# Kernel tuning notes

Measured on AMD Instinct MI355X. Metric: run time of the kernel, lower is better.

The kernel has to match this reference:

```python
import jax, jax.numpy as jnp
import numpy as np
from jax import lax

NUM_CHANNELS = 64
DILATION_DEPTH = 9
NUM_REPEAT = 2
KERNEL_SIZE = 3
DILATIONS = [2 ** d for d in range(DILATION_DEPTH)] * NUM_REPEAT  # 18 layers
B, T = 4, 32768


def causal_conv1d(x, w, b, dilation):
    # x: [B, Cin, T], w: [Cout, Cin, K], b: [Cout]
    # left-pad by (K-1)*dilation -> causal, output length T
    pad = (w.shape[-1] - 1) * dilation
    out = lax.conv_general_dilated(
        x, w, window_strides=(1,), padding=[(pad, 0)],
        rhs_dilation=(dilation,), dimension_numbers=("NCH", "OIH", "NCH"))
    return out + b[None, :, None]


def setup_inputs() -> dict:
    key = jax.random.key(0)
    ks = jax.random.split(key, 9)
    L, C = len(DILATIONS), NUM_CHANNELS
    s = 0.05
    return {
        "x": jax.random.normal(ks[0], (B, 1, T), dtype=jnp.float32),
        "in_w": jax.random.normal(ks[1], (C, 1, 1), dtype=jnp.float32) * s,
        "in_b": jax.random.normal(ks[2], (C,), dtype=jnp.float32) * s,
        "hid_w": jax.random.normal(ks[3], (L, 2 * C, C, KERNEL_SIZE), dtype=jnp.float32) * s,
        "hid_b": jax.random.normal(ks[4], (L, 2 * C), dtype=jnp.float32) * s,
        "res_w": jax.random.normal(ks[5], (L, C, C, 1), dtype=jnp.float32) * s,
        "res_b": jax.random.normal(ks[6], (L, C), dtype=jnp.float32) * s,
        "mix_w": jax.random.normal(ks[7], (1, L * C, 1), dtype=jnp.float32) * s,
        "mix_b": jax.random.normal(ks[8], (1,), dtype=jnp.float32) * s,
    }


def reference(x, in_w, in_b, hid_w, hid_b, res_w, res_b, mix_w, mix_b):
    C = NUM_CHANNELS
    out = causal_conv1d(x, in_w, in_b, 1)  # [B, C, T]
    skips = []
    for i, d in enumerate(DILATIONS):
        inp = out
        h = causal_conv1d(inp, hid_w[i], hid_b[i], d)  # [B, 2C, T]
        gated = jnp.tanh(h[:, :C]) * jax.nn.sigmoid(h[:, C:])  # [B, C, T]
        skips.append(gated)
        out = causal_conv1d(gated, res_w[i], res_b[i], 1) + inp
    skip_cat = jnp.concatenate(skips, axis=1)  # [B, L*C, T]
    return causal_conv1d(skip_cat, mix_w, mix_b, 1)  # [B, 1, T]
```

## Files before the change

kernel.cpp:

```cpp
#include <hip/hip_runtime.h>
#include <math.h>

#define T_LEN 32768
#define NB 4
#define NC 64
#define NL 18

typedef __attribute__((ext_vector_type(8))) short s16x8;
typedef __attribute__((ext_vector_type(4))) float f32x4;
#define MFMA_F16 __builtin_amdgcn_mfma_f32_16x16x32_f16

#define BAR_LGKM()                                                   \
    do {                                                             \
        asm volatile("s_waitcnt lgkmcnt(0)" ::: "memory");           \
        __builtin_amdgcn_s_barrier();                                \
        __builtin_amdgcn_sched_barrier(0);                           \
    } while (0)
#define BAR_VM(N)                                                    \
    do {                                                             \
        asm volatile("s_waitcnt vmcnt(%0) lgkmcnt(0)" ::             \
                         "i"(N) : "memory");                         \
        __builtin_amdgcn_s_barrier();                                \
        __builtin_amdgcn_sched_barrier(0);                           \
    } while (0)

__device__ inline unsigned short f2h(float f) {
    _Float16 h = (_Float16)f;
    return __builtin_bit_cast(unsigned short, h);
}
__device__ inline unsigned pack_h2(float a, float b) {
    return (unsigned)f2h(a) | ((unsigned)f2h(b) << 16);
}
__device__ inline float h2f(unsigned short u) {
    return (float)__builtin_bit_cast(_Float16, u);
}
__device__ inline float fast_sigmoid(float x) {
    return __builtin_amdgcn_rcpf(1.f + __expf(-x));
}
__device__ inline float fast_tanh(float x) {
    return 1.f - 2.f * __builtin_amdgcn_rcpf(1.f + __expf(2.f * x));
}

__global__ void prep_kernel(const float* __restrict__ hid_w,
                            const float* __restrict__ res_w,
                            const float* __restrict__ mix_b,
                            unsigned short* __restrict__ Wh,
                            unsigned short* __restrict__ Wr,
                            float* __restrict__ out,
                            float* __restrict__ zerobuf) {
    const int nW1 = NL * 128 * 192;
    const int nW2 = NL * 64 * 64;
    const int nOut = NB * T_LEN;
    const int total = nW1 + nW2 + nOut + 48;
    for (int gid = blockIdx.x * blockDim.x + threadIdx.x; gid < total;
         gid += gridDim.x * blockDim.x) {
        if (gid < nW1) {
            int K = gid % 192;
            int co = (gid / 192) & 127;
            int i = gid / (192 * 128);
            int kt = K >> 6, ci = K & 63;
            Wh[gid] = f2h(hid_w[((i * 128 + co) * 64 + ci) * 3 + kt]);
        } else if (gid < nW1 + nW2) {
            int q = gid - nW1;
            int c = q & 63, co = (q >> 6) & 63, i = q >> 12;
            Wr[q] = f2h(res_w[(i * 64 + co) * 64 + c]);
        } else if (gid < nW1 + nW2 + nOut) {
            out[gid - (nW1 + nW2)] = mix_b[0];
        } else {
            zerobuf[gid - (nW1 + nW2 + nOut)] = 0.f;
        }
    }
}

template <int DIL, bool FIRST, bool LAST>
__launch_bounds__(256, 4)
__global__ void layer_kernel(const unsigned short* __restrict__ actH,
                             unsigned short* __restrict__ outH,
                             const unsigned short* __restrict__ Wh,
                             const float* __restrict__ hb,
                             const unsigned short* __restrict__ Wr,
                             const float* __restrict__ rb,
                             const float* __restrict__ mw,
                             float* __restrict__ skip,
                             const float* __restrict__ zerobuf,
                             const float* __restrict__ x,
                             const float* __restrict__ in_w,
                             const float* __restrict__ in_b) {
    constexpr bool UNI = (DIL < 64);
    constexpr int R = UNI ? (64 + 2 * DIL) : 192;
    constexpr int SLOTS = R * 8;
    constexpr int JMAX = (SLOTS + 255) / 256;
    constexpr int GS_BASE = (UNI ? 128 : 0) * 128;
    constexpr int OUT_BASE = (UNI ? 0 : 64) * 128;
    constexpr int REG = 24576;

    __shared__ uint4 Xs[2 * 1536];
    __shared__ float Sk[256];
    char* lds = (char*)Xs;

    const int tid = threadIdx.x;
    const int w = tid >> 6;
    const int l = tid & 63;
    const int lo = l & 15;
    const int hi = l >> 4;
    const int blk = blockIdx.x;
    const int tile = (blk & 7) * 64 + (blk >> 3);
    const int t0 = tile * 64;
    const int m0 = 16 * w;
    const int c0 = m0 + 4 * hi;

    const float* xB0 = x;

    s16x8 AH[2][6];
    s16x8 AR[2];
#pragma unroll
    for (int mt = 0; mt < 2; mt++) {
        const unsigned short* wp = Wh + (size_t)(m0 + 64 * mt + lo) * 192;
#pragma unroll
        for (int s = 0; s < 6; s++)
            AH[mt][s] = *(const s16x8*)(wp + 32 * s + 8 * hi);
    }
    if (!LAST) {
#pragma unroll
        for (int s = 0; s < 2; s++)
            AR[s] = *(const s16x8*)(Wr + (size_t)(m0 + lo) * 64 + 32 * s + 8 * hi);
    }
    float bA[4], bB[4], rbv[4];
#pragma unroll
    for (int r = 0; r < 4; r++) {
        bA[r] = hb[c0 + r];
        bB[r] = hb[64 + c0 + r];
        rbv[r] = LAST ? 0.f : rb[c0 + r];
    }
    const float4 mw4 = *(const float4*)(mw + c0);

    auto stage_async = [&](int bb, char* X) {
        const unsigned short* aB = actH + (size_t)bb * T_LEN * NC;
#pragma unroll
        for (int jj = 0; jj < JMAX; jj++) {
            int s = (w * JMAX + jj) * 64 + l;
            const void* src;
            if (s >= SLOTS) {
                src = (const void*)(zerobuf + (s & 7) * 4);
            } else {
                int row = s >> 3, ch = s & 7;
                int chunk = ch ^ (row & 7);
                int tg = t0 + (UNI ? (row - 2 * DIL)
                                   : (((row >> 6) - 2) * DIL + (row & 63)));
                src = (tg >= 0)
                          ? (const void*)(aB + (size_t)tg * 64 + chunk * 8)
                          : (const void*)(zerobuf + chunk * 4);
            }
            __builtin_amdgcn_global_load_lds(
                (const __attribute__((address_space(1))) unsigned int*)src,
                (__attribute__((address_space(3))) unsigned int*)(X +
                                                        (w * JMAX + jj) * 1024),
                16, 0, 0);
        }
    };
    auto stage_first = [&](int bb, char* X) {
        const float* xB = xB0 + (size_t)bb * T_LEN;
#pragma unroll
        for (int jj = 0; jj < JMAX; jj++) {
            int p = jj * 256 + tid;
            if (p < SLOTS) {
                int row = p >> 3, ch = p & 7;
                int tg = t0 + row - 2 * DIL;
                unsigned uu[4] = {0u, 0u, 0u, 0u};
                if (tg >= 0) {
                    float a = xB[tg];
#pragma unroll
                    for (int e = 0; e < 4; e++) {
                        float v0 = a * in_w[ch * 8 + 2 * e] + in_b[ch * 8 + 2 * e];
                        float v1 = a * in_w[ch * 8 + 2 * e + 1] + in_b[ch * 8 + 2 * e + 1];
                        uu[e] = pack_h2(v0, v1);
                    }
                }
                int byte = (row * 128 + ch * 16) ^ ((row & 7) << 4);
                *(uint4*)(X + byte) = make_uint4(uu[0], uu[1], uu[2], uu[3]);
            }
        }
    };

    if (FIRST) stage_first(0, lds);
    else       stage_async(0, lds);

#pragma unroll
    for (int j = 0; j < NB; j++) {
        char* X = lds + (j & 1) * REG;
        const int b = j;

        if (j + 1 < NB) {
            if (FIRST) stage_first(j + 1, lds + ((j + 1) & 1) * REG);
            else       stage_async(j + 1, lds + ((j + 1) & 1) * REG);
        }

        if (FIRST)           { BAR_LGKM(); }
        else if (j + 1 < NB) { BAR_VM(JMAX); }
        else                 { BAR_VM(0); }

        f32x4 acc[2][4];
#pragma unroll
        for (int mt = 0; mt < 2; mt++)
#pragma unroll
            for (int nt = 0; nt < 4; nt++)
                acc[mt][nt] = (f32x4){0.f, 0.f, 0.f, 0.f};
        __builtin_amdgcn_s_setprio(1);
#pragma unroll
        for (int s = 0; s < 6; s++) {
            const int tap = s >> 1, half = s & 1;
#pragma unroll
            for (int nt = 0; nt < 4; nt++) {
                int t = 16 * nt + lo;
                int row = UNI ? (t + tap * DIL) : (tap * 64 + t);
                int byte = (row * 128 + half * 64 + hi * 16) ^ ((row & 7) << 4);
                s16x8 bx = __builtin_bit_cast(s16x8, *(const uint4*)(X + byte));
                acc[0][nt] = MFMA_F16(AH[0][s], bx, acc[0][nt], 0, 0, 0);
                acc[1][nt] = MFMA_F16(AH[1][s], bx, acc[1][nt], 0, 0, 0);
            }
        }
        __builtin_amdgcn_s_setprio(0);

        float4 inp[4];
        if (!LAST) {
#pragma unroll
            for (int nt = 0; nt < 4; nt++) {
                int t = 16 * nt + lo;
                int rowI = UNI ? (t + 2 * DIL) : (128 + t);
                int byteI = (rowI * 128 + c0 * 2) ^ ((rowI & 7) << 4);
                uint2 hv = *(const uint2*)(X + byteI);
                inp[nt] = make_float4(h2f((unsigned short)(hv.x & 0xffff)),
                                      h2f((unsigned short)(hv.x >> 16)),
                                      h2f((unsigned short)(hv.y & 0xffff)),
                                      h2f((unsigned short)(hv.y >> 16)));
            }
        }

        BAR_LGKM();

#pragma unroll
        for (int nt = 0; nt < 4; nt++) {
            float g[4];
#pragma unroll
            for (int r = 0; r < 4; r++) {
                float hA = acc[0][nt][r] + bA[r];
                float hB = acc[1][nt][r] + bB[r];
                g[r] = fast_tanh(hA) * fast_sigmoid(hB);
            }
            int t = 16 * nt + lo;
            if (!LAST) {
                int byte = (t * 128 + c0 * 2) ^ ((t & 7) << 4);
                *(uint2*)(X + GS_BASE + byte) =
                    make_uint2(pack_h2(g[0], g[1]), pack_h2(g[2], g[3]));
            }
            float sk = g[0] * mw4.x + g[1] * mw4.y + g[2] * mw4.z + g[3] * mw4.w;
            sk += __shfl_xor(sk, 16, 64);
            sk += __shfl_xor(sk, 32, 64);
            if (hi == 0) Sk[w * 64 + nt * 16 + lo] = sk;
        }
        BAR_LGKM();

        if (LAST) {
            if (tid < 64) {
                float s2 = Sk[tid] + Sk[64 + tid] + Sk[128 + tid] + Sk[192 + tid];
                skip[(size_t)b * T_LEN + t0 + tid] += s2;
            }
            BAR_LGKM();
            continue;
        }

        f32x4 acc2[4];
#pragma unroll
        for (int nt = 0; nt < 4; nt++) acc2[nt] = (f32x4){0.f, 0.f, 0.f, 0.f};
        __builtin_amdgcn_s_setprio(1);
#pragma unroll
        for (int s = 0; s < 2; s++) {
#pragma unroll
            for (int nt = 0; nt < 4; nt++) {
                int t = 16 * nt + lo;
                int byte = (t * 128 + s * 64 + hi * 16) ^ ((t & 7) << 4);
                s16x8 bg = __builtin_bit_cast(
                    s16x8, *(const uint4*)(X + GS_BASE + byte));
                acc2[nt] = MFMA_F16(AR[s], bg, acc2[nt], 0, 0, 0);
            }
        }
        __builtin_amdgcn_s_setprio(0);

        char* OutH = X + OUT_BASE;
#pragma unroll
        for (int nt = 0; nt < 4; nt++) {
            int t = 16 * nt + lo;
            float ox = acc2[nt][0] + rbv[0] + inp[nt].x;
            float oy = acc2[nt][1] + rbv[1] + inp[nt].y;
            float oz = acc2[nt][2] + rbv[2] + inp[nt].z;
            float ow = acc2[nt][3] + rbv[3] + inp[nt].w;
            int byteB = (t * 128 + c0 * 2) ^ ((t & 7) << 4);
            *(uint2*)(OutH + byteB) =
                make_uint2(pack_h2(ox, oy), pack_h2(oz, ow));
        }

        if (tid < 64) {
            float s2 = Sk[tid] + Sk[64 + tid] + Sk[128 + tid] + Sk[192 + tid];
            skip[(size_t)b * T_LEN + t0 + tid] += s2;
        }
        BAR_LGKM();

        unsigned short* gH = outH + (size_t)b * T_LEN * NC + (size_t)t0 * 64;
#pragma unroll
        for (int i = 0; i < 2; i++) {
            int u = i * 256 + tid;
            int t = u >> 3, ch = u & 7;
            uint4 v = *(const uint4*)(OutH + t * 128 + ((ch ^ (t & 7)) << 4));
            ((uint4*)gH)[u] = v;
        }
        BAR_LGKM();
    }
}

extern "C" void kernel_launch(void* const* d_in, const int* in_sizes, int n_in,
                              void* d_out, int out_size, void* d_ws, size_t ws_size,
                              hipStream_t stream) {
    const float* x     = (const float*)d_in[0];
    const float* in_w  = (const float*)d_in[1];
    const float* in_b  = (const float*)d_in[2];
    const float* hid_w = (const float*)d_in[3];
    const float* hid_b = (const float*)d_in[4];
    const float* res_w = (const float*)d_in[5];
    const float* res_b = (const float*)d_in[6];
    const float* mix_w = (const float*)d_in[7];
    const float* mix_b = (const float*)d_in[8];
    float* out = (float*)d_out;

    const size_t actN = (size_t)NB * T_LEN * NC;
    unsigned short* H0 = (unsigned short*)d_ws;
    unsigned short* H1 = H0 + actN;
    unsigned short* Wh = H1 + actN;
    unsigned short* Wr = Wh + (size_t)NL * 128 * 192;
    float* zerobuf = (float*)(Wr + (size_t)NL * 64 * 64);

    prep_kernel<<<512, 256, 0, stream>>>(hid_w, res_w, mix_b, Wh, Wr, out,
                                         zerobuf);

    static const int dils[NL] = {1, 2, 4, 8, 16, 32, 64, 128, 256,
                                 1, 2, 4, 8, 16, 32, 64, 128, 256};
    const unsigned short* srcH = H0;
    unsigned short* dstH = H1;

#define LL(D, F, L)                                                           \
    layer_kernel<D, F, L><<<512, 256, 0, stream>>>(                           \
        srcH, dstH, Wh + (size_t)i * 128 * 192, hid_b + (size_t)i * 128,      \
        Wr + (size_t)i * 64 * 64, res_b + (size_t)i * 64,                     \
        mix_w + (size_t)i * 64, out, zerobuf, x, in_w, in_b)

    for (int i = 0; i < NL; i++) {
        if (i == 0) {
            LL(1, true, false);
        } else if (i == NL - 1) {
            LL(256, false, true);
        } else {
            switch (dils[i]) {
                case 1:   LL(1, false, false);   break;
                case 2:   LL(2, false, false);   break;
                case 4:   LL(4, false, false);   break;
                case 8:   LL(8, false, false);   break;
                case 16:  LL(16, false, false);  break;
                case 32:  LL(32, false, false);  break;
                case 64:  LL(64, false, false);  break;
                case 128: LL(128, false, false); break;
                case 256: LL(256, false, false); break;
            }
        }
        const unsigned short* tH = srcH; srcH = dstH; dstH = (unsigned short*)tH;
    }
#undef LL
}
```

Baseline: 347.1 us.

## Fuse all layers into one persistent kernel with per-tile progress flags

Replaces the 18 per-layer launches with a single persistent kernel over 512 tiles. Each tile waits on atomic progress counters of neighbouring tiles (left for the causal receptive field, right for the ping-pong buffer overwrite) before running the next layer. This removes launch gaps and global layer barriers, letting tiles proceed as soon as their dependencies are ready. It relies on all 512 blocks being co-resident and on a bounded spin-wait, and it changes the tile-to-block mapping and the first/last flags from compile-time to runtime.

```diff
diff --git a/kernel.cpp b/kernel.cpp
--- a/kernel.cpp
+++ b/kernel.cpp
@@ -5,6 +5,7 @@
 #define NB 4
 #define NC 64
 #define NL 18
+#define NTILE 512
 
 typedef __attribute__((ext_vector_type(8))) short s16x8;
 typedef __attribute__((ext_vector_type(4))) float f32x4;
@@ -41,6 +42,15 @@
     return 1.f - 2.f * __builtin_amdgcn_rcpf(1.f + __expf(2.f * x));
 }
 
+__device__ inline void wait_ge(unsigned* p, unsigned v) {
+    for (int it = 0; it < (1 << 16); ++it) {
+        unsigned cur = __hip_atomic_load(p, __ATOMIC_ACQUIRE,
+                                         __HIP_MEMORY_SCOPE_AGENT);
+        if (cur >= v) return;
+        __builtin_amdgcn_s_sleep(16);
+    }
+}
+
 __global__ void prep_kernel(const float* __restrict__ hid_w,
                             const float* __restrict__ res_w,
                             const float* __restrict__ mix_b,
@@ -51,7 +61,7 @@
     const int nW1 = NL * 128 * 192;
     const int nW2 = NL * 64 * 64;
     const int nOut = NB * T_LEN;
-    const int total = nW1 + nW2 + nOut + 48;
+    const int total = nW1 + nW2 + nOut + 32 + NTILE;
     for (int gid = blockIdx.x * blockDim.x + threadIdx.x; gid < total;
          gid += gridDim.x * blockDim.x) {
         if (gid < nW1) {
@@ -72,20 +82,17 @@
     }
 }
 
-template <int DIL, bool FIRST, bool LAST>
-__launch_bounds__(256, 4)
-__global__ void layer_kernel(const unsigned short* __restrict__ actH,
-                             unsigned short* __restrict__ outH,
-                             const unsigned short* __restrict__ Wh,
-                             const float* __restrict__ hb,
-                             const unsigned short* __restrict__ Wr,
-                             const float* __restrict__ rb,
-                             const float* __restrict__ mw,
-                             float* __restrict__ skip,
-                             const float* __restrict__ zerobuf,
-                             const float* __restrict__ x,
-                             const float* __restrict__ in_w,
-                             const float* __restrict__ in_b) {
+template <int DIL>
+__device__ __forceinline__ void layer_body(
+    const bool first, const bool last,
+    const unsigned short* actH, unsigned short* outH,
+    const unsigned short* Wh, const float* hb,
+    const unsigned short* Wr, const float* rb,
+    const float* mw, float* skip,
+    const float* zerobuf, const float* x,
+    const float* in_w, const float* in_b,
+    char* lds, float* Sk, const int t0)
+{
     constexpr bool UNI = (DIL < 64);
     constexpr int R = UNI ? (64 + 2 * DIL) : 192;
     constexpr int SLOTS = R * 8;
@@ -94,23 +101,14 @@
     constexpr int OUT_BASE = (UNI ? 0 : 64) * 128;
     constexpr int REG = 24576;
 
-    __shared__ uint4 Xs[2 * 1536];
-    __shared__ float Sk[256];
-    char* lds = (char*)Xs;
-
     const int tid = threadIdx.x;
     const int w = tid >> 6;
     const int l = tid & 63;
     const int lo = l & 15;
     const int hi = l >> 4;
-    const int blk = blockIdx.x;
-    const int tile = (blk & 7) * 64 + (blk >> 3);
-    const int t0 = tile * 64;
     const int m0 = 16 * w;
     const int c0 = m0 + 4 * hi;
 
-    const float* xB0 = x;
-
     s16x8 AH[2][6];
     s16x8 AR[2];
 #pragma unroll
@@ -120,7 +118,7 @@
         for (int s = 0; s < 6; s++)
             AH[mt][s] = *(const s16x8*)(wp + 32 * s + 8 * hi);
     }
-    if (!LAST) {
+    if (!(DIL == 256 && last)) {
 #pragma unroll
         for (int s = 0; s < 2; s++)
             AR[s] = *(const s16x8*)(Wr + (size_t)(m0 + lo) * 64 + 32 * s + 8 * hi);
@@ -130,7 +128,7 @@
     for (int r = 0; r < 4; r++) {
         bA[r] = hb[c0 + r];
         bB[r] = hb[64 + c0 + r];
-        rbv[r] = LAST ? 0.f : rb[c0 + r];
+        rbv[r] = (DIL == 256 && last) ? 0.f : rb[c0 + r];
     }
     const float4 mw4 = *(const float4*)(mw + c0);
 
@@ -159,7 +157,7 @@
         }
     };
     auto stage_first = [&](int bb, char* X) {
-        const float* xB = xB0 + (size_t)bb * T_LEN;
+        const float* xB = x + (size_t)bb * T_LEN;
 #pragma unroll
         for (int jj = 0; jj < JMAX; jj++) {
             int p = jj * 256 + tid;
@@ -182,8 +180,8 @@
         }
     };
 
-    if (FIRST) stage_first(0, lds);
-    else       stage_async(0, lds);
+    if (DIL == 1 && first) stage_first(0, lds);
+    else                   stage_async(0, lds);
 
 #pragma unroll
     for (int j = 0; j < NB; j++) {
@@ -191,13 +189,13 @@
         const int b = j;
 
         if (j + 1 < NB) {
-            if (FIRST) stage_first(j + 1, lds + ((j + 1) & 1) * REG);
-            else       stage_async(j + 1, lds + ((j + 1) & 1) * REG);
-        }
-
-        if (FIRST)           { BAR_LGKM(); }
-        else if (j + 1 < NB) { BAR_VM(JMAX); }
-        else                 { BAR_VM(0); }
+            if (DIL == 1 && first) stage_first(j + 1, lds + ((j + 1) & 1) * REG);
+            else                   stage_async(j + 1, lds + ((j + 1) & 1) * REG);
+        }
+
+        if (DIL == 1 && first) { BAR_LGKM(); }
+        else if (j + 1 < NB)   { BAR_VM(JMAX); }
+        else                   { BAR_VM(0); }
 
         f32x4 acc[2][4];
 #pragma unroll
@@ -222,7 +220,7 @@
         __builtin_amdgcn_s_setprio(0);
 
         float4 inp[4];
-        if (!LAST) {
+        if (!(DIL == 256 && last)) {
 #pragma unroll
             for (int nt = 0; nt < 4; nt++) {
                 int t = 16 * nt + lo;
@@ -248,7 +246,7 @@
                 g[r] = fast_tanh(hA) * fast_sigmoid(hB);
             }
             int t = 16 * nt + lo;
-            if (!LAST) {
+            if (!(DIL == 256 && last)) {
                 int byte = (t * 128 + c0 * 2) ^ ((t & 7) << 4);
                 *(uint2*)(X + GS_BASE + byte) =
                     make_uint2(pack_h2(g[0], g[1]), pack_h2(g[2], g[3]));
@@ -260,7 +258,7 @@
         }
         BAR_LGKM();
 
-        if (LAST) {
+        if (DIL == 256 && last) {
             if (tid < 64) {
                 float s2 = Sk[tid] + Sk[64 + tid] + Sk[128 + tid] + Sk[192 + tid];
                 skip[(size_t)b * T_LEN + t0 + tid] += s2;
@@ -315,6 +313,77 @@
         }
         BAR_LGKM();
     }
+}
+
+__launch_bounds__(256, 4)
+__global__ void mega_kernel(unsigned short* H0, unsigned short* H1,
+                            const unsigned short* Wh, const float* hid_b,
+                            const unsigned short* Wr, const float* res_b,
+                            const float* mix_w, float* out,
+                            const float* zerobuf, const float* x,
+                            const float* in_w, const float* in_b,
+                            unsigned* prog)
+{
+    __shared__ uint4 Xs[2 * 1536];
+    __shared__ float Sk[256];
+    char* lds = (char*)Xs;
+
+    const int tid = threadIdx.x;
+    const int tile = blockIdx.x;
+    const int t0 = tile * 64;
+
+    unsigned short* src = H0;
+    unsigned short* dst = H1;
+    int L = 0;
+    int prevspan = 0;
+
+#define SPAN(D) ((D) < 64 ? 1 : (D) / 32)
+#define LSTEP(D)                                                             \
+    {                                                                        \
+        const bool first = (L == 0);                                         \
+        const bool last = (L == NL - 1);                                     \
+        if (tid == 0) {                                                      \
+            if (!first) {                                                    \
+                for (int s = 1; s <= SPAN(D); ++s) {                         \
+                    int tt = tile - s;                                       \
+                    if (tt < 0) break;                                       \
+                    wait_ge(prog + tt, (unsigned)L);                         \
+                }                                                            \
+            }                                                                \
+            if (L >= 2) {                                                    \
+                for (int s = 1; s <= prevspan; ++s) {                        \
+                    int tt = tile + s;                                       \
+                    if (tt >= NTILE) break;                                  \
+                    wait_ge(prog + tt, (unsigned)L);                         \
+                }                                                            \
+            }                                                                \
+        }                                                                    \
+        __syncthreads();                                                     \
+        layer_body<D>(first, last, src, dst, Wh + (size_t)L * 128 * 192,     \
+                      hid_b + L * 128, Wr + (size_t)L * 64 * 64,             \
+                      res_b + L * 64, mix_w + L * 64, out, zerobuf, x,       \
+                      in_w, in_b, lds, Sk, t0);                              \
+        if (!last) {                                                         \
+            asm volatile("s_waitcnt vmcnt(0) lgkmcnt(0)" ::: "memory");      \
+            __syncthreads();                                                 \
+            if (tid == 0)                                                    \
+                __hip_atomic_store(prog + tile, (unsigned)(L + 1),           \
+                                   __ATOMIC_RELEASE,                         \
+                                   __HIP_MEMORY_SCOPE_AGENT);                \
+            unsigned short* tswap = src;                                     \
+            src = dst;                                                       \
+            dst = tswap;                                                     \
+        }                                                                    \
+        prevspan = SPAN(D);                                                  \
+        ++L;                                                                 \
+    }
+
+    LSTEP(1) LSTEP(2) LSTEP(4) LSTEP(8) LSTEP(16)
+    LSTEP(32) LSTEP(64) LSTEP(128) LSTEP(256)
+    LSTEP(1) LSTEP(2) LSTEP(4) LSTEP(8) LSTEP(16)
+    LSTEP(32) LSTEP(64) LSTEP(128) LSTEP(256)
+#undef LSTEP
+#undef SPAN
 }
 
 extern "C" void kernel_launch(void* const* d_in, const int* in_sizes, int n_in,
@@ -337,40 +406,12 @@
     unsigned short* Wh = H1 + actN;
     unsigned short* Wr = Wh + (size_t)NL * 128 * 192;
     float* zerobuf = (float*)(Wr + (size_t)NL * 64 * 64);
+    unsigned* prog = (unsigned*)(zerobuf + 32);
 
     prep_kernel<<<512, 256, 0, stream>>>(hid_w, res_w, mix_b, Wh, Wr, out,
                                          zerobuf);
 
-    static const int dils[NL] = {1, 2, 4, 8, 16, 32, 64, 128, 256,
-                                 1, 2, 4, 8, 16, 32, 64, 128, 256};
-    const unsigned short* srcH = H0;
-    unsigned short* dstH = H1;
-
-#define LL(D, F, L)                                                           \
-    layer_kernel<D, F, L><<<512, 256, 0, stream>>>(                           \
-        srcH, dstH, Wh + (size_t)i * 128 * 192, hid_b + (size_t)i * 128,      \
-        Wr + (size_t)i * 64 * 64, res_b + (size_t)i * 64,                     \
-        mix_w + (size_t)i * 64, out, zerobuf, x, in_w, in_b)
-
-    for (int i = 0; i < NL; i++) {
-        if (i == 0) {
-            LL(1, true, false);
-        } else if (i == NL - 1) {
-            LL(256, false, true);
-        } else {
-            switch (dils[i]) {
-                case 1:   LL(1, false, false);   break;
-                case 2:   LL(2, false, false);   break;
-                case 4:   LL(4, false, false);   break;
-                case 8:   LL(8, false, false);   break;
-                case 16:  LL(16, false, false);  break;
-                case 32:  LL(32, false, false);  break;
-                case 64:  LL(64, false, false);  break;
-                case 128: LL(128, false, false); break;
-                case 256: LL(256, false, false); break;
-            }
-        }
-        const unsigned short* tH = srcH; srcH = dstH; dstH = (unsigned short*)tH;
-    }
-#undef LL
-}
+    mega_kernel<<<NTILE, 256, 0, stream>>>(H0, H1, Wh, hid_b, Wr, res_b,
+                                           mix_w, out, zerobuf, x, in_w, in_b,
+                                           prog);
+}
```

After: 1.166 ms. 3.36x slower.

## Fuse consecutive small-dilation layer pairs into one kernel with halo recompute

Applied to the files above, without the earlier changes.

Adds a pair_kernel that runs two consecutive WaveNet layers in one launch. It stages an extended halo so layer A's output for the 16 extra rows that layer B's dilated taps need is computed in LDS. Layer pairs (4,8), (1,2), (4,8) now use it, removing one global write and read of the activation tensor plus one launch per pair. The cost is redundant halo compute, more registers for two weight sets, and more LDS per block.

```diff
diff --git a/kernel.cpp b/kernel.cpp
--- a/kernel.cpp
+++ b/kernel.cpp
@@ -317,6 +317,310 @@
     }
 }
 
+template <int DA, int DB>
+__launch_bounds__(256, 2)
+__global__ void pair_kernel(const unsigned short* __restrict__ actH,
+                            unsigned short* __restrict__ outH,
+                            const unsigned short* __restrict__ WhA,
+                            const float* __restrict__ hbA,
+                            const unsigned short* __restrict__ WrA,
+                            const float* __restrict__ rbA,
+                            const float* __restrict__ mwA,
+                            const unsigned short* __restrict__ WhB,
+                            const float* __restrict__ hbB,
+                            const unsigned short* __restrict__ WrB,
+                            const float* __restrict__ rbB,
+                            const float* __restrict__ mwB,
+                            float* __restrict__ skip,
+                            const float* __restrict__ zerobuf) {
+    constexpr int R = 80 + 2 * DA;
+    constexpr int SLOTS = R * 8;
+    constexpr int JMAX = (SLOTS + 255) / 256;
+    constexpr int REG = 12288;
+
+    __shared__ uint4 Xs[2 * 768];
+    __shared__ uint4 OutA[640];
+    __shared__ uint4 GsB[512];
+    __shared__ float Sk[256];
+    char* lds = (char*)Xs;
+    char* outa = (char*)OutA;
+    char* gsb = (char*)GsB;
+
+    const int tid = threadIdx.x;
+    const int w = tid >> 6;
+    const int l = tid & 63;
+    const int lo = l & 15;
+    const int hi = l >> 4;
+    const int blk = blockIdx.x;
+    const int tile = (blk & 7) * 64 + (blk >> 3);
+    const int t0 = tile * 64;
+    const int m0 = 16 * w;
+    const int c0 = m0 + 4 * hi;
+
+    s16x8 AHa[2][6], ARa[2], AHb[2][6], ARb[2];
+#pragma unroll
+    for (int mt = 0; mt < 2; mt++) {
+        const unsigned short* wa = WhA + (size_t)(m0 + 64 * mt + lo) * 192;
+        const unsigned short* wb = WhB + (size_t)(m0 + 64 * mt + lo) * 192;
+#pragma unroll
+        for (int s = 0; s < 6; s++) {
+            AHa[mt][s] = *(const s16x8*)(wa + 32 * s + 8 * hi);
+            AHb[mt][s] = *(const s16x8*)(wb + 32 * s + 8 * hi);
+        }
+    }
+#pragma unroll
+    for (int s = 0; s < 2; s++) {
+        ARa[s] = *(const s16x8*)(WrA + (size_t)(m0 + lo) * 64 + 32 * s + 8 * hi);
+        ARb[s] = *(const s16x8*)(WrB + (size_t)(m0 + lo) * 64 + 32 * s + 8 * hi);
+    }
+    float bAa[4], bBa[4], rva[4], bAb[4], bBb[4], rvb[4];
+#pragma unroll
+    for (int r = 0; r < 4; r++) {
+        bAa[r] = hbA[c0 + r];
+        bBa[r] = hbA[64 + c0 + r];
+        rva[r] = rbA[c0 + r];
+        bAb[r] = hbB[c0 + r];
+        bBb[r] = hbB[64 + c0 + r];
+        rvb[r] = rbB[c0 + r];
+    }
+    const float4 mw4a = *(const float4*)(mwA + c0);
+    const float4 mw4b = *(const float4*)(mwB + c0);
+
+    auto stage = [&](int bb, char* X) {
+        const unsigned short* aB = actH + (size_t)bb * T_LEN * NC;
+#pragma unroll
+        for (int jj = 0; jj < JMAX; jj++) {
+            int s = (w * JMAX + jj) * 64 + l;
+            const void* src;
+            if (s >= SLOTS) {
+                src = (const void*)(zerobuf + (s & 7) * 4);
+            } else {
+                int row = s >> 3, ch = s & 7;
+                int chunk = ch ^ (row & 7);
+                int tg = t0 - 16 - 2 * DA + row;
+                src = (tg >= 0)
+                          ? (const void*)(aB + (size_t)tg * 64 + chunk * 8)
+                          : (const void*)(zerobuf + chunk * 4);
+            }
+            __builtin_amdgcn_global_load_lds(
+                (const __attribute__((address_space(1))) unsigned int*)src,
+                (__attribute__((address_space(3))) unsigned int*)(X +
+                                                        (w * JMAX + jj) * 1024),
+                16, 0, 0);
+        }
+    };
+
+    stage(0, lds);
+
+#pragma unroll
+    for (int j = 0; j < NB; j++) {
+        char* X = lds + (j & 1) * REG;
+        const int b = j;
+
+        if (j + 1 < NB) stage(j + 1, lds + ((j + 1) & 1) * REG);
+
+        if (j + 1 < NB) { BAR_VM(JMAX); }
+        else            { BAR_VM(0); }
+
+        f32x4 acc[2][5];
+#pragma unroll
+        for (int mt = 0; mt < 2; mt++)
+#pragma unroll
+            for (int nt = 0; nt < 5; nt++)
+                acc[mt][nt] = (f32x4){0.f, 0.f, 0.f, 0.f};
+        __builtin_amdgcn_s_setprio(1);
+#pragma unroll
+        for (int s = 0; s < 6; s++) {
+            const int tap = s >> 1, half = s & 1;
+#pragma unroll
+            for (int nt = 0; nt < 5; nt++) {
+                int e = 16 * nt + lo;
+                int row = e + tap * DA;
+                int byte = (row * 128 + half * 64 + hi * 16) ^ ((row & 7) << 4);
+                s16x8 bx = __builtin_bit_cast(s16x8, *(const uint4*)(X + byte));
+                acc[0][nt] = MFMA_F16(AHa[0][s], bx, acc[0][nt], 0, 0, 0);
+                acc[1][nt] = MFMA_F16(AHa[1][s], bx, acc[1][nt], 0, 0, 0);
+            }
+        }
+        __builtin_amdgcn_s_setprio(0);
+
+        float4 inpa[5];
+#pragma unroll
+        for (int nt = 0; nt < 5; nt++) {
+            int e = 16 * nt + lo;
+            int rowI = e + 2 * DA;
+            int byteI = (rowI * 128 + c0 * 2) ^ ((rowI & 7) << 4);
+            uint2 hv = *(const uint2*)(X + byteI);
+            inpa[nt] = make_float4(h2f((unsigned short)(hv.x & 0xffff)),
+                                   h2f((unsigned short)(hv.x >> 16)),
+                                   h2f((unsigned short)(hv.y & 0xffff)),
+                                   h2f((unsigned short)(hv.y >> 16)));
+        }
+
+        BAR_LGKM();
+
+#pragma unroll
+        for (int nt = 0; nt < 5; nt++) {
+            float g[4];
+#pragma unroll
+            for (int r = 0; r < 4; r++) {
+                float hA = acc[0][nt][r] + bAa[r];
+                float hB = acc[1][nt][r] + bBa[r];
+                g[r] = fast_tanh(hA) * fast_sigmoid(hB);
+            }
+            int e = 16 * nt + lo;
+            int byte = (e * 128 + c0 * 2) ^ ((e & 7) << 4);
+            *(uint2*)(X + byte) =
+                make_uint2(pack_h2(g[0], g[1]), pack_h2(g[2], g[3]));
+            if (nt >= 1) {
+                float sk = g[0] * mw4a.x + g[1] * mw4a.y + g[2] * mw4a.z +
+                           g[3] * mw4a.w;
+                sk += __shfl_xor(sk, 16, 64);
+                sk += __shfl_xor(sk, 32, 64);
+                if (hi == 0) Sk[w * 64 + (nt - 1) * 16 + lo] = sk;
+            }
+        }
+        BAR_LGKM();
+
+        f32x4 acc2[5];
+#pragma unroll
+        for (int nt = 0; nt < 5; nt++) acc2[nt] = (f32x4){0.f, 0.f, 0.f, 0.f};
+        __builtin_amdgcn_s_setprio(1);
+#pragma unroll
+        for (int s = 0; s < 2; s++) {
+#pragma unroll
+            for (int nt = 0; nt < 5; nt++) {
+                int e = 16 * nt + lo;
+                int byte = (e * 128 + s * 64 + hi * 16) ^ ((e & 7) << 4);
+                s16x8 bg = __builtin_bit_cast(s16x8, *(const uint4*)(X + byte));
+                acc2[nt] = MFMA_F16(ARa[s], bg, acc2[nt], 0, 0, 0);
+            }
+        }
+        __builtin_amdgcn_s_setprio(0);
+
+#pragma unroll
+        for (int nt = 0; nt < 5; nt++) {
+            int e = 16 * nt + lo;
+            int tg_a = t0 - 16 + e;
+            float ox = acc2[nt][0] + rva[0] + inpa[nt].x;
+            float oy = acc2[nt][1] + rva[1] + inpa[nt].y;
+            float oz = acc2[nt][2] + rva[2] + inpa[nt].z;
+            float ow = acc2[nt][3] + rva[3] + inpa[nt].w;
+            if (tg_a < 0) { ox = 0.f; oy = 0.f; oz = 0.f; ow = 0.f; }
+            int byte = (e * 128 + c0 * 2) ^ ((e & 7) << 4);
+            *(uint2*)(outa + byte) =
+                make_uint2(pack_h2(ox, oy), pack_h2(oz, ow));
+        }
+        if (tid < 64) {
+            float s2 = Sk[tid] + Sk[64 + tid] + Sk[128 + tid] + Sk[192 + tid];
+            skip[(size_t)b * T_LEN + t0 + tid] += s2;
+        }
+        BAR_LGKM();
+
+        f32x4 accb[2][4];
+#pragma unroll
+        for (int mt = 0; mt < 2; mt++)
+#pragma unroll
+            for (int nt = 0; nt < 4; nt++)
+                accb[mt][nt] = (f32x4){0.f, 0.f, 0.f, 0.f};
+        __builtin_amdgcn_s_setprio(1);
+#pragma unroll
+        for (int s = 0; s < 6; s++) {
+            const int tap = s >> 1, half = s & 1;
+#pragma unroll
+            for (int nt = 0; nt < 4; nt++) {
+                int u = 16 * nt + lo;
+                int row = u + 16 + (tap - 2) * DB;
+                int byte = (row * 128 + half * 64 + hi * 16) ^ ((row & 7) << 4);
+                s16x8 bx =
+                    __builtin_bit_cast(s16x8, *(const uint4*)(outa + byte));
+                accb[0][nt] = MFMA_F16(AHb[0][s], bx, accb[0][nt], 0, 0, 0);
+                accb[1][nt] = MFMA_F16(AHb[1][s], bx, accb[1][nt], 0, 0, 0);
+            }
+        }
+        __builtin_amdgcn_s_setprio(0);
+
+        float4 inpb[4];
+#pragma unroll
+        for (int nt = 0; nt < 4; nt++) {
+            int u = 16 * nt + lo;
+            int rowI = u + 16;
+            int byteI = (rowI * 128 + c0 * 2) ^ ((rowI & 7) << 4);
+            uint2 hv = *(const uint2*)(outa + byteI);
+            inpb[nt] = make_float4(h2f((unsigned short)(hv.x & 0xffff)),
+                                   h2f((unsigned short)(hv.x >> 16)),
+                                   h2f((unsigned short)(hv.y & 0xffff)),
+                                   h2f((unsigned short)(hv.y >> 16)));
+        }
+
+#pragma unroll
+        for (int nt = 0; nt < 4; nt++) {
+            float g[4];
+#pragma unroll
+            for (int r = 0; r < 4; r++) {
+                float hA = accb[0][nt][r] + bAb[r];
+                float hB = accb[1][nt][r] + bBb[r];
+                g[r] = fast_tanh(hA) * fast_sigmoid(hB);
+            }
+            int u = 16 * nt + lo;
+            int byte = (u * 128 + c0 * 2) ^ ((u & 7) << 4);
+            *(uint2*)(gsb + byte) =
+                make_uint2(pack_h2(g[0], g[1]), pack_h2(g[2], g[3]));
+            float sk = g[0] * mw4b.x + g[1] * mw4b.y + g[2] * mw4b.z +
+                       g[3] * mw4b.w;
+            sk += __shfl_xor(sk, 16, 64);
+            sk += __shfl_xor(sk, 32, 64);
+            if (hi == 0) Sk[w * 64 + nt * 16 + lo] = sk;
+        }
+        BAR_LGKM();
+
+        f32x4 acc2b[4];
+#pragma unroll
+        for (int nt = 0; nt < 4; nt++) acc2b[nt] = (f32x4){0.f, 0.f, 0.f, 0.f};
+        __builtin_amdgcn_s_setprio(1);
+#pragma unroll
+        for (int s = 0; s < 2; s++) {
+#pragma unroll
+            for (int nt = 0; nt < 4; nt++) {
+                int u = 16 * nt + lo;
+                int byte = (u * 128 + s * 64 + hi * 16) ^ ((u & 7) << 4);
+                s16x8 bg =
+                    __builtin_bit_cast(s16x8, *(const uint4*)(gsb + byte));
+                acc2b[nt] = MFMA_F16(ARb[s], bg, acc2b[nt], 0, 0, 0);
+            }
+        }
+        __builtin_amdgcn_s_setprio(0);
+
+        char* OutB = X;
+#pragma unroll
+        for (int nt = 0; nt < 4; nt++) {
+            int u = 16 * nt + lo;
+            float ox = acc2b[nt][0] + rvb[0] + inpb[nt].x;
+            float oy = acc2b[nt][1] + rvb[1] + inpb[nt].y;
+            float oz = acc2b[nt][2] + rvb[2] + inpb[nt].z;
+            float ow = acc2b[nt][3] + rvb[3] + inpb[nt].w;
+            int byte = (u * 128 + c0 * 2) ^ ((u & 7) << 4);
+            *(uint2*)(OutB + byte) =
+                make_uint2(pack_h2(ox, oy), pack_h2(oz, ow));
+        }
+        if (tid < 64) {
+            float s2 = Sk[tid] + Sk[64 + tid] + Sk[128 + tid] + Sk[192 + tid];
+            skip[(size_t)b * T_LEN + t0 + tid] += s2;
+        }
+        BAR_LGKM();
+
+        unsigned short* gH = outH + (size_t)b * T_LEN * NC + (size_t)t0 * 64;
+#pragma unroll
+        for (int i = 0; i < 2; i++) {
+            int u = i * 256 + tid;
+            int t = u >> 3, ch = u & 7;
+            uint4 v = *(const uint4*)(OutB + t * 128 + ((ch ^ (t & 7)) << 4));
+            ((uint4*)gH)[u] = v;
+        }
+        BAR_LGKM();
+    }
+}
+
 extern "C" void kernel_launch(void* const* d_in, const int* in_sizes, int n_in,
                               void* d_out, int out_size, void* d_ws, size_t ws_size,
                               hipStream_t stream) {
@@ -341,36 +645,44 @@
     prep_kernel<<<512, 256, 0, stream>>>(hid_w, res_w, mix_b, Wh, Wr, out,
                                          zerobuf);
 
-    static const int dils[NL] = {1, 2, 4, 8, 16, 32, 64, 128, 256,
-                                 1, 2, 4, 8, 16, 32, 64, 128, 256};
     const unsigned short* srcH = H0;
     unsigned short* dstH = H1;
 
-#define LL(D, F, L)                                                           \
+#define SWAP()                                                                \
+    do {                                                                      \
+        const unsigned short* tH = srcH;                                      \
+        srcH = dstH;                                                          \
+        dstH = (unsigned short*)tH;                                           \
+    } while (0)
+#define LL(D, F, L, i)                                                        \
     layer_kernel<D, F, L><<<512, 256, 0, stream>>>(                           \
-        srcH, dstH, Wh + (size_t)i * 128 * 192, hid_b + (size_t)i * 128,      \
-        Wr + (size_t)i * 64 * 64, res_b + (size_t)i * 64,                     \
-        mix_w + (size_t)i * 64, out, zerobuf, x, in_w, in_b)
-
-    for (int i = 0; i < NL; i++) {
-        if (i == 0) {
-            LL(1, true, false);
-        } else if (i == NL - 1) {
-            LL(256, false, true);
-        } else {
-            switch (dils[i]) {
-                case 1:   LL(1, false, false);   break;
-                case 2:   LL(2, false, false);   break;
-                case 4:   LL(4, false, false);   break;
-                case 8:   LL(8, false, false);   break;
-                case 16:  LL(16, false, false);  break;
-                case 32:  LL(32, false, false);  break;
-                case 64:  LL(64, false, false);  break;
-                case 128: LL(128, false, false); break;
-                case 256: LL(256, false, false); break;
-            }
-        }
-        const unsigned short* tH = srcH; srcH = dstH; dstH = (unsigned short*)tH;
-    }
+        srcH, dstH, Wh + (size_t)(i) * 128 * 192, hid_b + (size_t)(i) * 128,  \
+        Wr + (size_t)(i) * 64 * 64, res_b + (size_t)(i) * 64,                 \
+        mix_w + (size_t)(i) * 64, out, zerobuf, x, in_w, in_b)
+#define LP(DA_, DB_, LA)                                                      \
+    pair_kernel<DA_, DB_><<<512, 256, 0, stream>>>(                           \
+        srcH, dstH, Wh + (size_t)(LA) * 128 * 192, hid_b + (LA) * 128,        \
+        Wr + (size_t)(LA) * 64 * 64, res_b + (LA) * 64, mix_w + (LA) * 64,    \
+        Wh + (size_t)(LA + 1) * 128 * 192, hid_b + (LA + 1) * 128,            \
+        Wr + (size_t)(LA + 1) * 64 * 64, res_b + (LA + 1) * 64,               \
+        mix_w + (LA + 1) * 64, out, zerobuf)
+
+    LL(1, true, false, 0);     SWAP();
+    LL(2, false, false, 1);    SWAP();
+    LP(4, 8, 2);               SWAP();
+    LL(16, false, false, 4);   SWAP();
+    LL(32, false, false, 5);   SWAP();
+    LL(64, false, false, 6);   SWAP();
+    LL(128, false, false, 7);  SWAP();
+    LL(256, false, false, 8);  SWAP();
+    LP(1, 2, 9);               SWAP();
+    LP(4, 8, 11);              SWAP();
+    LL(16, false, false, 13);  SWAP();
+    LL(32, false, false, 14);  SWAP();
+    LL(64, false, false, 15);  SWAP();
+    LL(128, false, false, 16); SWAP();
+    LL(256, false, true, 17);
+#undef LP
 #undef LL
-}
+#undef SWAP
+}
```

Result: slower. 414.9 us (+19.5%).
